# Optimization experiments

Hardware: AMD Instinct MI355X
Metric: run time of the kernel (lower is better)

The kernel has to match this reference:

```python
import jax, jax.numpy as jnp
import numpy as np

N_NODES = 32768
N_EDGES = 262144
B = 64
FT_IN = 256
HID = 256
HEADS = 4
C = HID // HEADS
FT_OUT = 256
NEG_SLOPE = 0.2


def _lin(k, fi, fo):
    return jax.random.normal(k, (fi, fo), dtype=jnp.float32) / np.sqrt(fi)


def setup_inputs() -> dict:
    key = jax.random.key(0)
    ks = jax.random.split(key, 20)
    x = jax.random.normal(ks[0], (N_NODES, FT_IN), dtype=jnp.float32)
    edge_index = jax.random.randint(ks[1], (2, N_EDGES), 0, N_NODES, dtype=jnp.int64)
    batch = jnp.repeat(jnp.arange(B, dtype=jnp.int64), N_NODES // B)  # sorted segment ids
    return {
        "x": x,
        "edge_index": edge_index,
        "batch": batch,
        "batch_size": B,
        "W1l": _lin(ks[2], FT_IN, HID),
        "W1r": _lin(ks[3], FT_IN, HID),
        "a1": jax.random.normal(ks[4], (HEADS, C), dtype=jnp.float32) / np.sqrt(C),
        "b1": jnp.zeros((HID,), dtype=jnp.float32),
        "W2l": _lin(ks[5], HID, HID),
        "W2r": _lin(ks[6], HID, HID),
        "a2": jax.random.normal(ks[7], (HEADS, C), dtype=jnp.float32) / np.sqrt(C),
        "b2": jnp.zeros((HID,), dtype=jnp.float32),
        "Wm1": _lin(ks[8], HID, 4 * HID),
        "bm1": jnp.zeros((4 * HID,), dtype=jnp.float32),
        "Wm2": _lin(ks[9], 4 * HID, HID),
        "bm2": jnp.zeros((HID,), dtype=jnp.float32),
        "Wf": _lin(ks[10], HID, FT_OUT),
        "bf": jnp.zeros((FT_OUT,), dtype=jnp.float32),
    }


def gatv2_layer(x, src, dst, Wl, Wr, att, bias):
    """PyG GATv2Conv (concat=True, add_self_loops=True, eval-mode dropout)."""
    n = x.shape[0]
    h, c = att.shape
    xl = (x @ Wl).reshape(n, h, c)  # source-side transform (x_j)
    xr = (x @ Wr).reshape(n, h, c)  # target-side transform (x_i)
    loop = jnp.arange(n, dtype=src.dtype)
    s = jnp.concatenate([src, loop])
    d = jnp.concatenate([dst, loop])
    # e_ij = a^T LeakyReLU(Wl x_j + Wr x_i), per head
    e = jax.nn.leaky_relu(xl[s] + xr[d], NEG_SLOPE)  # [E+N, H, C]
    score = jnp.einsum('ehc,hc->eh', e, att)  # [E+N, H]
    # segment softmax over incoming edges of each dst node
    m = jax.ops.segment_max(score, d, num_segments=n)
    ex = jnp.exp(score - m[d])
    denom = jax.ops.segment_sum(ex, d, num_segments=n)
    alpha = ex / denom[d]  # self-loops guarantee denom > 0
    out = jax.ops.segment_sum(alpha[..., None] * xl[s], d, num_segments=n)
    return out.reshape(n, h * c) + bias


def _gelu(x):
    return jax.nn.gelu(x, approximate=False)


def reference(x, edge_index, batch, batch_size,
              W1l, W1r, a1, b1, W2l, W2r, a2, b2,
              Wm1, bm1, Wm2, bm2, Wf, bf):
    src, dst = edge_index[0], edge_index[1]
    h = _gelu(gatv2_layer(x, src, dst, W1l, W1r, a1, b1))
    h = _gelu(gatv2_layer(h, src, dst, W2l, W2r, a2, b2))
    # global mean pool over graphs
    cnt = jax.ops.segment_sum(jnp.ones((h.shape[0],), h.dtype), batch, num_segments=batch_size)
    graph_mean = jax.ops.segment_sum(h, batch, num_segments=batch_size) / cnt[:, None]
    # root node of each graph (node 0 of each contiguous block)
    root = h.reshape(batch_size, -1, h.shape[-1])[:, 0, :]
    z = _gelu(root @ Wm1 + bm1)
    z = _gelu(z @ Wm2 + bm2)
    out = z @ Wf + bf
    return (out, graph_mean)
```

## Files before the change

kernel.cpp:

```cpp
#include <hip/hip_runtime.h>
#include <math.h>

#define NNODES 32768
#define BGRAPH 64
#define NPG 512
#define HID 256

typedef __bf16 bf16x8 __attribute__((ext_vector_type(8)));
typedef float f32x16 __attribute__((ext_vector_type(16)));
typedef unsigned short ushort_t;
typedef unsigned short ushort8v __attribute__((ext_vector_type(8)));
typedef unsigned short ushort4v __attribute__((ext_vector_type(4)));
typedef _Float16 half4v __attribute__((ext_vector_type(4)));

__device__ __forceinline__ float gelu_f(float x) {
  return 0.5f * x * (1.0f + erff(x * 0.70710678118654752440f));
}

__device__ __forceinline__ int swz_off(int r, int k) {
  int kblk = k & ~63;
  int ch = (k >> 3) & 7;
  int slot = ch ^ (r & 7);
  return r * 256 + kblk + (slot << 3) + (k & 7);
}

__device__ __forceinline__ void gll16(const void* g, void* l) {
  __builtin_amdgcn_global_load_lds(
      (const __attribute__((address_space(1))) unsigned int*)g,
      (__attribute__((address_space(3))) unsigned int*)l, 16, 0, 0);
}

__device__ __forceinline__ float dpp_sum16(float x) {
  int t;
  t = __builtin_amdgcn_update_dpp(0, __builtin_bit_cast(int, x), 0xB1, 0xF, 0xF, true);
  x += __builtin_bit_cast(float, t);
  t = __builtin_amdgcn_update_dpp(0, __builtin_bit_cast(int, x), 0x4E, 0xF, 0xF, true);
  x += __builtin_bit_cast(float, t);
  t = __builtin_amdgcn_update_dpp(0, __builtin_bit_cast(int, x), 0x141, 0xF, 0xF, true);
  x += __builtin_bit_cast(float, t);
  t = __builtin_amdgcn_update_dpp(0, __builtin_bit_cast(int, x), 0x140, 0xF, 0xF, true);
  x += __builtin_bit_cast(float, t);
  return x;
}

__global__ __launch_bounds__(256) void prep_kernel(
    const int* __restrict__ src, const int* __restrict__ dst, int E,
    int* __restrict__ cnt, ushort_t* __restrict__ col_pad,
    const float* __restrict__ W1l, const float* __restrict__ W1r,
    const float* __restrict__ W2l, const float* __restrict__ W2r,
    ushort_t* __restrict__ B1h, ushort_t* __restrict__ B1l,
    ushort_t* __restrict__ B2h, ushort_t* __restrict__ B2l,
    const float* __restrict__ x,
    ushort_t* __restrict__ Xh, ushort_t* __restrict__ Xl) {
  int b = blockIdx.x;
  if (b < 1024) {
    int e = b * 256 + threadIdx.x;
    if (e < E) {
      int d = dst[e];
      int slot = atomicAdd(&cnt[d], 1);
      if (slot < 64) col_pad[(d << 6) | slot] = (ushort_t)src[e];
    }
  } else if (b < 1152) {
    int idx = (b - 1024) * 256 + threadIdx.x;
    int layer = idx >> 14;
    int n = (idx >> 5) & 511;
    int c32 = idx & 31;
    const float* W = layer ? (n < 256 ? W2l : W2r) : (n < 256 ? W1l : W1r);
    int wn = n & 255;
    ushort8v hv, lv;
#pragma unroll
    for (int j = 0; j < 8; ++j) {
      float v = W[(size_t)(c32 * 8 + j) * 256 + wn];
      __bf16 h = (__bf16)v;
      float rem = v - (float)h;
      __bf16 l = (__bf16)rem;
      hv[j] = __builtin_bit_cast(ushort_t, h);
      lv[j] = __builtin_bit_cast(ushort_t, l);
    }
    int off = swz_off(n, c32 * 8);
    ushort_t* ho = layer ? B2h : B1h;
    ushort_t* lo = layer ? B2l : B1l;
    *(ushort8v*)(ho + off) = hv;
    *(ushort8v*)(lo + off) = lv;
  } else {
    int idx = (b - 1152) * 256 + threadIdx.x;
    int r = idx >> 5;
    int c32 = idx & 31;
    const float* srcp = x + (size_t)r * 256 + c32 * 8;
    float4 v0 = *(const float4*)srcp;
    float4 v1 = *(const float4*)(srcp + 4);
    float vv[8] = {v0.x, v0.y, v0.z, v0.w, v1.x, v1.y, v1.z, v1.w};
    ushort8v hv, lv;
#pragma unroll
    for (int j = 0; j < 8; ++j) {
      __bf16 h = (__bf16)vv[j];
      float rem = vv[j] - (float)h;
      __bf16 l = (__bf16)rem;
      hv[j] = __builtin_bit_cast(ushort_t, h);
      lv[j] = __builtin_bit_cast(ushort_t, l);
    }
    int off = swz_off(r, c32 * 8);
    *(ushort8v*)(Xh + off) = hv;
    *(ushort8v*)(Xl + off) = lv;
  }
}

__global__ __launch_bounds__(256, 2) void gemm_bf16x3(
    const ushort_t* __restrict__ Ahi, const ushort_t* __restrict__ Alo,
    const ushort_t* __restrict__ Bhi, const ushort_t* __restrict__ Blo,
    _Float16* __restrict__ Cl, float* __restrict__ Cr) {
  __shared__ ushort_t lds[4 * 128 * 64];
  int i = blockIdx.x;
  int xcd = i & 7, slot = i >> 3;
  int bm = (xcd * 32 + (slot >> 2)) * 128;
  int bn = (slot & 3) * 128;

  int tid = threadIdx.x;
  int w = tid >> 6, lane = tid & 63;
  int r = lane & 31, kg = lane >> 5;

  const ushort_t* gsrc = (w == 0) ? Ahi : (w == 1) ? Alo : (w == 2) ? Bhi : Blo;
  int rowbase = (w < 2) ? bm : bn;
  const ushort_t* gptr = gsrc + (size_t)(rowbase + (lane >> 3)) * 256 + (lane & 7) * 8;
  ushort_t* ldsw = lds + w * (128 * 64) + lane * 8;

  int wm0 = (w >> 1) * 64, wn0 = (w & 1) * 64;

  f32x16 acc[2][2];
#pragma unroll
  for (int mf = 0; mf < 2; ++mf)
#pragma unroll
    for (int nf = 0; nf < 2; ++nf)
#pragma unroll
      for (int e = 0; e < 16; ++e) acc[mf][nf][e] = 0.0f;

  for (int kk = 0; kk < 256; kk += 64) {
#pragma unroll
    for (int t = 0; t < 16; ++t)
      gll16(gptr + (size_t)t * 2048 + kk, ldsw + t * 512);
    __syncthreads();

#pragma unroll
    for (int ks = 0; ks < 4; ++ks) {
      int so = (((ks << 1) | kg) ^ (r & 7)) << 3;
      bf16x8 ah[2], al[2], bh[2], bl[2];
#pragma unroll
      for (int mf = 0; mf < 2; ++mf) {
        int rb = (wm0 + mf * 32 + r) * 64 + so;
        ah[mf] = *(const bf16x8*)(lds + rb);
        al[mf] = *(const bf16x8*)(lds + 8192 + rb);
      }
#pragma unroll
      for (int nf = 0; nf < 2; ++nf) {
        int rb = (wn0 + nf * 32 + r) * 64 + so;
        bh[nf] = *(const bf16x8*)(lds + 16384 + rb);
        bl[nf] = *(const bf16x8*)(lds + 24576 + rb);
      }
#pragma unroll
      for (int mf = 0; mf < 2; ++mf)
#pragma unroll
        for (int nf = 0; nf < 2; ++nf) {
          acc[mf][nf] = __builtin_amdgcn_mfma_f32_32x32x16_bf16(ah[mf], bh[nf], acc[mf][nf], 0, 0, 0);
          acc[mf][nf] = __builtin_amdgcn_mfma_f32_32x32x16_bf16(ah[mf], bl[nf], acc[mf][nf], 0, 0, 0);
          acc[mf][nf] = __builtin_amdgcn_mfma_f32_32x32x16_bf16(al[mf], bh[nf], acc[mf][nf], 0, 0, 0);
        }
    }
    __syncthreads();
  }

#pragma unroll
  for (int mf = 0; mf < 2; ++mf)
#pragma unroll
    for (int nf = 0; nf < 2; ++nf) {
      int colbase = bn + wn0 + nf * 32;
      int cn = (colbase + r) & 255;
#pragma unroll
      for (int g = 0; g < 16; ++g) {
        int row = bm + wm0 + mf * 32 + (g & 3) + ((g >> 2) << 3) + (kg << 2);
        if (colbase < 256)
          Cl[(size_t)row * 256 + cn] = (_Float16)acc[mf][nf][g];
        else
          Cr[(size_t)row * 256 + cn] = acc[mf][nf][g];
      }
    }
}

__global__ __launch_bounds__(256) void gat_agg(const _Float16* __restrict__ xl,
                                               const float* __restrict__ xr,
                                               const float* __restrict__ att,
                                               const float* __restrict__ bias,
                                               const int* __restrict__ cnt,
                                               const ushort_t* __restrict__ col_pad,
                                               ushort_t* __restrict__ hi_out,
                                               ushort_t* __restrict__ lo_out,
                                               _Float16* __restrict__ h2f16,
                                               float* __restrict__ rootbuf) {
  int wave = (int)((blockIdx.x * (size_t)blockDim.x + threadIdx.x) >> 6);
  int lane = threadIdx.x & 63;
  int d = wave;
  int c0 = lane * 4;
  float4 xr4 = *(const float4*)(xr + (size_t)d * HID + c0);
  float4 a4 = *(const float4*)(att + c0);
  int deg = cnt[d];
  deg = deg < 64 ? deg : 64;
  int mycol = (int)col_pad[(d << 6) + lane];

  auto loadrow = [&](int j) -> float4 {
    int s = (j < deg) ? __builtin_amdgcn_readlane(mycol, j) : d;
    half4v hv = *(const half4v*)(xl + (size_t)s * HID + c0);
    return make_float4((float)hv[0], (float)hv[1], (float)hv[2], (float)hv[3]);
  };

  float l = 0.f, A0 = 0.f, A1 = 0.f, A2 = 0.f, A3 = 0.f;
  float4 v = loadrow(0);
  for (int j = 0; j <= deg; ++j) {
    float4 vc = v;
    if (j < deg) v = loadrow(j + 1);
    float t0 = vc.x + xr4.x, t1 = vc.y + xr4.y, t2 = vc.z + xr4.z, t3 = vc.w + xr4.w;
    t0 = fmaf(0.4f, fabsf(t0), 0.6f * t0);
    t1 = fmaf(0.4f, fabsf(t1), 0.6f * t1);
    t2 = fmaf(0.4f, fabsf(t2), 0.6f * t2);
    t3 = fmaf(0.4f, fabsf(t3), 0.6f * t3);
    float sc = a4.x * t0;
    sc = fmaf(a4.y, t1, sc);
    sc = fmaf(a4.z, t2, sc);
    sc = fmaf(a4.w, t3, sc);
    sc = dpp_sum16(sc);
    float p = __expf(sc);
    l += p;
    A0 = fmaf(p, vc.x, A0);
    A1 = fmaf(p, vc.y, A1);
    A2 = fmaf(p, vc.z, A2);
    A3 = fmaf(p, vc.w, A3);
  }

  float inv = 1.0f / l;
  float v0 = gelu_f(fmaf(A0, inv, bias[c0 + 0]));
  float v1 = gelu_f(fmaf(A1, inv, bias[c0 + 1]));
  float v2 = gelu_f(fmaf(A2, inv, bias[c0 + 2]));
  float v3 = gelu_f(fmaf(A3, inv, bias[c0 + 3]));

  if (hi_out) {
    float vv[4] = {v0, v1, v2, v3};
    ushort4v hv, lv;
#pragma unroll
    for (int j = 0; j < 4; ++j) {
      __bf16 h = (__bf16)vv[j];
      float rem = vv[j] - (float)h;
      __bf16 lb = (__bf16)rem;
      hv[j] = __builtin_bit_cast(ushort_t, h);
      lv[j] = __builtin_bit_cast(ushort_t, lb);
    }
    int off = swz_off(d, c0);
    *(ushort4v*)(hi_out + off) = hv;
    *(ushort4v*)(lo_out + off) = lv;
  }
  if (h2f16) {
    half4v o;
    o[0] = (_Float16)v0; o[1] = (_Float16)v1; o[2] = (_Float16)v2; o[3] = (_Float16)v3;
    *(half4v*)(h2f16 + (size_t)d * HID + c0) = o;
    if ((d & (NPG - 1)) == 0)
      *(float4*)(rootbuf + (size_t)(d >> 9) * HID + c0) = make_float4(v0, v1, v2, v3);
  }
}

__global__ __launch_bounds__(256) void pool_kernel(const _Float16* __restrict__ h2,
                                                   float* __restrict__ gmean) {
  int g = blockIdx.x >> 2;
  int q = blockIdx.x & 3;
  int c = threadIdx.x;
  const _Float16* p = h2 + ((size_t)g * NPG + q * 128) * HID + c;
  float s = 0.f;
#pragma unroll 4
  for (int i = 0; i < 128; ++i) s += (float)p[(size_t)i * HID];
  atomicAdd(&gmean[(size_t)g * HID + c], s * (1.0f / (float)NPG));
}

template <int KIN, int NOUT, int NCHUNK, bool GELU>
__global__ __launch_bounds__(256) void mlp_kernel(const float* __restrict__ in, size_t row_stride,
                                                  const float* __restrict__ W,
                                                  const float* __restrict__ b,
                                                  float* __restrict__ outp) {
  __shared__ float s_in[KIN];
  int g = blockIdx.x / NCHUNK;
  int n0 = (blockIdx.x % NCHUNK) * (NOUT / NCHUNK);
  const float* row = in + (size_t)g * row_stride;
  for (int i = threadIdx.x; i < KIN; i += 256) s_in[i] = row[i];
  __syncthreads();
  constexpr int CPT = NOUT / NCHUNK / 256;
  float acc[CPT] = {};
  for (int k = 0; k < KIN; ++k) {
    float a = s_in[k];
#pragma unroll
    for (int j = 0; j < CPT; ++j) acc[j] += a * W[(size_t)k * NOUT + n0 + threadIdx.x + j * 256];
  }
#pragma unroll
  for (int j = 0; j < CPT; ++j) {
    float v = acc[j] + b[n0 + threadIdx.x + j * 256];
    if (GELU) v = gelu_f(v);
    outp[(size_t)g * NOUT + n0 + threadIdx.x + j * 256] = v;
  }
}

extern "C" void kernel_launch(void* const* d_in, const int* in_sizes, int n_in,
                              void* d_out, int out_size, void* d_ws, size_t ws_size,
                              hipStream_t stream) {
  const float* x   = (const float*)d_in[0];
  const int* edge  = (const int*)d_in[1];
  const float* W1l = (const float*)d_in[4];
  const float* W1r = (const float*)d_in[5];
  const float* a1  = (const float*)d_in[6];
  const float* b1  = (const float*)d_in[7];
  const float* W2l = (const float*)d_in[8];
  const float* W2r = (const float*)d_in[9];
  const float* a2  = (const float*)d_in[10];
  const float* b2  = (const float*)d_in[11];
  const float* Wm1 = (const float*)d_in[12];
  const float* bm1 = (const float*)d_in[13];
  const float* Wm2 = (const float*)d_in[14];
  const float* bm2 = (const float*)d_in[15];
  const float* Wf  = (const float*)d_in[16];
  const float* bf  = (const float*)d_in[17];
  float* out = (float*)d_out;
  float* gmean = out + BGRAPH * HID;

  const int n = NNODES;
  const int E = in_sizes[1] / 2;
  const int* src = edge;
  const int* dst = edge + E;

  ushort_t* R1h = (ushort_t*)d_ws;
  ushort_t* R1l = R1h + (size_t)n * 256;
  _Float16* h2f16 = (_Float16*)R1h;
  _Float16* xlh = (_Float16*)(R1l + (size_t)n * 256);
  float* xrbuf = (float*)(xlh + (size_t)n * 256);
  float* rootbuf = xrbuf + (size_t)n * 256;
  float* z1 = rootbuf + 64 * 256;
  float* z2 = z1 + 64 * 1024;
  ushort_t* B1h = (ushort_t*)(z2 + 64 * 256);
  ushort_t* B1l = B1h + 512 * 256;
  ushort_t* B2h = B1l + 512 * 256;
  ushort_t* B2l = B2h + 512 * 256;
  int* cnt = (int*)(B2l + 512 * 256);
  ushort_t* col_pad = (ushort_t*)(cnt + n);

  hipMemsetAsync(cnt, 0, (size_t)n * sizeof(int), stream);
  hipMemsetAsync(gmean, 0, (size_t)BGRAPH * HID * sizeof(float), stream);

  prep_kernel<<<1024 + 128 + 4096, 256, 0, stream>>>(
      src, dst, E, cnt, col_pad, W1l, W1r, W2l, W2r,
      B1h, B1l, B2h, B2l, x, R1h, R1l);

  gemm_bf16x3<<<1024, 256, 0, stream>>>(R1h, R1l, B1h, B1l, xlh, xrbuf);
  gat_agg<<<n / 4, 256, 0, stream>>>(xlh, xrbuf, a1, b1, cnt, col_pad,
                                     R1h, R1l, nullptr, nullptr);
  gemm_bf16x3<<<1024, 256, 0, stream>>>(R1h, R1l, B2h, B2l, xlh, xrbuf);
  gat_agg<<<n / 4, 256, 0, stream>>>(xlh, xrbuf, a2, b2, cnt, col_pad,
                                     nullptr, nullptr, h2f16, rootbuf);

  pool_kernel<<<BGRAPH * 4, 256, 0, stream>>>(h2f16, gmean);
  mlp_kernel<256, 1024, 4, true><<<BGRAPH * 4, 256, 0, stream>>>(rootbuf, 256, Wm1, bm1, z1);
  mlp_kernel<1024, 256, 1, true><<<BGRAPH, 256, 0, stream>>>(z1, 1024, Wm2, bm2, z2);
  mlp_kernel<256, 256, 1, false><<<BGRAPH, 256, 0, stream>>>(z2, 256, Wf, bf, out);
}
```

Baseline: 330.4 us.

## Store GEMM operands in MFMA fragment order and load directly from global

Producers now write the bf16 hi/lo operands in a layout that matches the MFMA 32x32x16 fragment order, so each lane loads its fragment with one contiguous 16-byte global read. The GEMM drops LDS staging, global_load_lds and the barriers, and raises launch bounds to 3 blocks per CU. This removes LDS traffic and sync, but each wave now reads its tiles from global/L2 with no sharing between waves in a block, which duplicates global traffic.

```diff
diff --git a/kernel.cpp b/kernel.cpp
--- a/kernel.cpp
+++ b/kernel.cpp
@@ -17,17 +17,9 @@
   return 0.5f * x * (1.0f + erff(x * 0.70710678118654752440f));
 }
 
-__device__ __forceinline__ int swz_off(int r, int k) {
-  int kblk = k & ~63;
-  int ch = (k >> 3) & 7;
-  int slot = ch ^ (r & 7);
-  return r * 256 + kblk + (slot << 3) + (k & 7);
-}
-
-__device__ __forceinline__ void gll16(const void* g, void* l) {
-  __builtin_amdgcn_global_load_lds(
-      (const __attribute__((address_space(1))) unsigned int*)g,
-      (__attribute__((address_space(3))) unsigned int*)l, 16, 0, 0);
+__device__ __forceinline__ size_t frag_off(int r, int k) {
+  return ((size_t)((r >> 5) * 16 + (k >> 4)) << 9) +
+         (size_t)(((r & 31) | (((k >> 3) & 1) << 5)) << 3) + (k & 7);
 }
 
 __device__ __forceinline__ float dpp_sum16(float x) {
@@ -77,7 +69,7 @@
       hv[j] = __builtin_bit_cast(ushort_t, h);
       lv[j] = __builtin_bit_cast(ushort_t, l);
     }
-    int off = swz_off(n, c32 * 8);
+    size_t off = frag_off(n, c32 * 8);
     ushort_t* ho = layer ? B2h : B1h;
     ushort_t* lo = layer ? B2l : B1l;
     *(ushort8v*)(ho + off) = hv;
@@ -99,32 +91,27 @@
       hv[j] = __builtin_bit_cast(ushort_t, h);
       lv[j] = __builtin_bit_cast(ushort_t, l);
     }
-    int off = swz_off(r, c32 * 8);
+    size_t off = frag_off(r, c32 * 8);
     *(ushort8v*)(Xh + off) = hv;
     *(ushort8v*)(Xl + off) = lv;
   }
 }
 
-__global__ __launch_bounds__(256, 2) void gemm_bf16x3(
+__global__ __launch_bounds__(256, 3) void gemm_bf16x3(
     const ushort_t* __restrict__ Ahi, const ushort_t* __restrict__ Alo,
     const ushort_t* __restrict__ Bhi, const ushort_t* __restrict__ Blo,
     _Float16* __restrict__ Cl, float* __restrict__ Cr) {
-  __shared__ ushort_t lds[4 * 128 * 64];
   int i = blockIdx.x;
   int xcd = i & 7, slot = i >> 3;
   int bm = (xcd * 32 + (slot >> 2)) * 128;
   int bn = (slot & 3) * 128;
 
-  int tid = threadIdx.x;
-  int w = tid >> 6, lane = tid & 63;
+  int w = threadIdx.x >> 6, lane = threadIdx.x & 63;
+  int wm0 = (w >> 1) * 64, wn0 = (w & 1) * 64;
   int r = lane & 31, kg = lane >> 5;
 
-  const ushort_t* gsrc = (w == 0) ? Ahi : (w == 1) ? Alo : (w == 2) ? Bhi : Blo;
-  int rowbase = (w < 2) ? bm : bn;
-  const ushort_t* gptr = gsrc + (size_t)(rowbase + (lane >> 3)) * 256 + (lane & 7) * 8;
-  ushort_t* ldsw = lds + w * (128 * 64) + lane * 8;
-
-  int wm0 = (w >> 1) * 64, wn0 = (w & 1) * 64;
+  int rb0 = (bm + wm0) >> 5;
+  int cb0 = (bn + wn0) >> 5;
 
   f32x16 acc[2][2];
 #pragma unroll
@@ -134,38 +121,29 @@
 #pragma unroll
       for (int e = 0; e < 16; ++e) acc[mf][nf][e] = 0.0f;
 
-  for (int kk = 0; kk < 256; kk += 64) {
-#pragma unroll
-    for (int t = 0; t < 16; ++t)
-      gll16(gptr + (size_t)t * 2048 + kk, ldsw + t * 512);
-    __syncthreads();
-
-#pragma unroll
-    for (int ks = 0; ks < 4; ++ks) {
-      int so = (((ks << 1) | kg) ^ (r & 7)) << 3;
-      bf16x8 ah[2], al[2], bh[2], bl[2];
-#pragma unroll
-      for (int mf = 0; mf < 2; ++mf) {
-        int rb = (wm0 + mf * 32 + r) * 64 + so;
-        ah[mf] = *(const bf16x8*)(lds + rb);
-        al[mf] = *(const bf16x8*)(lds + 8192 + rb);
+#pragma unroll
+  for (int kq = 0; kq < 16; ++kq) {
+    bf16x8 ah[2], al[2], bh[2], bl[2];
+#pragma unroll
+    for (int mf = 0; mf < 2; ++mf) {
+      size_t o = ((size_t)((rb0 + mf) * 16 + kq) << 9) + (lane << 3);
+      ah[mf] = *(const bf16x8*)(Ahi + o);
+      al[mf] = *(const bf16x8*)(Alo + o);
+    }
+#pragma unroll
+    for (int nf = 0; nf < 2; ++nf) {
+      size_t o = ((size_t)((cb0 + nf) * 16 + kq) << 9) + (lane << 3);
+      bh[nf] = *(const bf16x8*)(Bhi + o);
+      bl[nf] = *(const bf16x8*)(Blo + o);
+    }
+#pragma unroll
+    for (int mf = 0; mf < 2; ++mf)
+#pragma unroll
+      for (int nf = 0; nf < 2; ++nf) {
+        acc[mf][nf] = __builtin_amdgcn_mfma_f32_32x32x16_bf16(ah[mf], bh[nf], acc[mf][nf], 0, 0, 0);
+        acc[mf][nf] = __builtin_amdgcn_mfma_f32_32x32x16_bf16(ah[mf], bl[nf], acc[mf][nf], 0, 0, 0);
+        acc[mf][nf] = __builtin_amdgcn_mfma_f32_32x32x16_bf16(al[mf], bh[nf], acc[mf][nf], 0, 0, 0);
       }
-#pragma unroll
-      for (int nf = 0; nf < 2; ++nf) {
-        int rb = (wn0 + nf * 32 + r) * 64 + so;
-        bh[nf] = *(const bf16x8*)(lds + 16384 + rb);
-        bl[nf] = *(const bf16x8*)(lds + 24576 + rb);
-      }
-#pragma unroll
-      for (int mf = 0; mf < 2; ++mf)
-#pragma unroll
-        for (int nf = 0; nf < 2; ++nf) {
-          acc[mf][nf] = __builtin_amdgcn_mfma_f32_32x32x16_bf16(ah[mf], bh[nf], acc[mf][nf], 0, 0, 0);
-          acc[mf][nf] = __builtin_amdgcn_mfma_f32_32x32x16_bf16(ah[mf], bl[nf], acc[mf][nf], 0, 0, 0);
-          acc[mf][nf] = __builtin_amdgcn_mfma_f32_32x32x16_bf16(al[mf], bh[nf], acc[mf][nf], 0, 0, 0);
-        }
-    }
-    __syncthreads();
   }
 
 #pragma unroll
@@ -251,7 +229,7 @@
       hv[j] = __builtin_bit_cast(ushort_t, h);
       lv[j] = __builtin_bit_cast(ushort_t, lb);
     }
-    int off = swz_off(d, c0);
+    size_t off = frag_off(d, c0);
     *(ushort4v*)(hi_out + off) = hv;
     *(ushort4v*)(lo_out + off) = lv;
   }
```

Result: no change. 329.9 us (-0.1%).

## Load GEMM weights as pre-laid MFMA fragments from global; fuse pool and MLP tail

Applied to the files above, without the earlier changes.

The weight matrices are now stored in an MFMA-fragment layout during prep. The GEMM reads the B operand straight from global (L2-resident) instead of staging it in LDS. This halves LDS use per block and raises the occupancy target to 3 blocks per SM. Separately, pooling now reduces inside a 1024-thread block without atomics, which removes the gmean memset, and the last two MLP layers are fused into one kernel to save a launch. The trade-off is that direct global B loads add latency inside the MFMA loop.

```diff
diff --git a/kernel.cpp b/kernel.cpp
--- a/kernel.cpp
+++ b/kernel.cpp
@@ -22,6 +22,11 @@
   int ch = (k >> 3) & 7;
   int slot = ch ^ (r & 7);
   return r * 256 + kblk + (slot << 3) + (k & 7);
+}
+
+__device__ __forceinline__ size_t frag_off(int r, int k) {
+  return ((size_t)((r >> 5) * 16 + (k >> 4)) << 9) +
+         (size_t)(((r & 31) | (((k >> 3) & 1) << 5)) << 3) + (k & 7);
 }
 
 __device__ __forceinline__ void gll16(const void* g, void* l) {
@@ -77,7 +82,7 @@
       hv[j] = __builtin_bit_cast(ushort_t, h);
       lv[j] = __builtin_bit_cast(ushort_t, l);
     }
-    int off = swz_off(n, c32 * 8);
+    size_t off = frag_off(n, c32 * 8);
     ushort_t* ho = layer ? B2h : B1h;
     ushort_t* lo = layer ? B2l : B1l;
     *(ushort8v*)(ho + off) = hv;
@@ -105,11 +110,11 @@
   }
 }
 
-__global__ __launch_bounds__(256, 2) void gemm_bf16x3(
+__global__ __launch_bounds__(256, 3) void gemm_bf16x3(
     const ushort_t* __restrict__ Ahi, const ushort_t* __restrict__ Alo,
     const ushort_t* __restrict__ Bhi, const ushort_t* __restrict__ Blo,
     _Float16* __restrict__ Cl, float* __restrict__ Cr) {
-  __shared__ ushort_t lds[4 * 128 * 64];
+  __shared__ ushort_t lds[2 * 8192];
   int i = blockIdx.x;
   int xcd = i & 7, slot = i >> 3;
   int bm = (xcd * 32 + (slot >> 2)) * 128;
@@ -117,14 +122,9 @@
 
   int tid = threadIdx.x;
   int w = tid >> 6, lane = tid & 63;
+  int wm0 = (w >> 1) * 64, wn0 = (w & 1) * 64;
   int r = lane & 31, kg = lane >> 5;
-
-  const ushort_t* gsrc = (w == 0) ? Ahi : (w == 1) ? Alo : (w == 2) ? Bhi : Blo;
-  int rowbase = (w < 2) ? bm : bn;
-  const ushort_t* gptr = gsrc + (size_t)(rowbase + (lane >> 3)) * 256 + (lane & 7) * 8;
-  ushort_t* ldsw = lds + w * (128 * 64) + lane * 8;
-
-  int wm0 = (w >> 1) * 64, wn0 = (w & 1) * 64;
+  int cb0 = (bn + wn0) >> 5;
 
   f32x16 acc[2][2];
 #pragma unroll
@@ -136,10 +136,16 @@
 
   for (int kk = 0; kk < 256; kk += 64) {
 #pragma unroll
-    for (int t = 0; t < 16; ++t)
-      gll16(gptr + (size_t)t * 2048 + kk, ldsw + t * 512);
+    for (int t = 0; t < 8; ++t) {
+      int tile = t >> 2;
+      int q = tid + (t & 3) * 256;
+      const ushort_t* gsrc = tile ? Alo : Ahi;
+      gll16(gsrc + (size_t)(bm + (q >> 3)) * 256 + kk + (q & 7) * 8,
+            lds + tile * 8192 + q * 8);
+    }
     __syncthreads();
 
+    int kq0 = kk >> 4;
 #pragma unroll
     for (int ks = 0; ks < 4; ++ks) {
       int so = (((ks << 1) | kg) ^ (r & 7)) << 3;
@@ -152,9 +158,9 @@
       }
 #pragma unroll
       for (int nf = 0; nf < 2; ++nf) {
-        int rb = (wn0 + nf * 32 + r) * 64 + so;
-        bh[nf] = *(const bf16x8*)(lds + 16384 + rb);
-        bl[nf] = *(const bf16x8*)(lds + 24576 + rb);
+        size_t o = ((size_t)((cb0 + nf) * 16 + kq0 + ks) << 9) + (lane << 3);
+        bh[nf] = *(const bf16x8*)(Bhi + o);
+        bl[nf] = *(const bf16x8*)(Blo + o);
       }
 #pragma unroll
       for (int mf = 0; mf < 2; ++mf)
@@ -264,42 +270,61 @@
   }
 }
 
-__global__ __launch_bounds__(256) void pool_kernel(const _Float16* __restrict__ h2,
-                                                   float* __restrict__ gmean) {
-  int g = blockIdx.x >> 2;
-  int q = blockIdx.x & 3;
-  int c = threadIdx.x;
+__global__ __launch_bounds__(1024) void pool_kernel(const _Float16* __restrict__ h2,
+                                                    float* __restrict__ gmean) {
+  __shared__ float buf[1024];
+  int g = blockIdx.x;
+  int q = threadIdx.x >> 8;
+  int c = threadIdx.x & 255;
   const _Float16* p = h2 + ((size_t)g * NPG + q * 128) * HID + c;
   float s = 0.f;
 #pragma unroll 4
   for (int i = 0; i < 128; ++i) s += (float)p[(size_t)i * HID];
-  atomicAdd(&gmean[(size_t)g * HID + c], s * (1.0f / (float)NPG));
-}
-
-template <int KIN, int NOUT, int NCHUNK, bool GELU>
-__global__ __launch_bounds__(256) void mlp_kernel(const float* __restrict__ in, size_t row_stride,
-                                                  const float* __restrict__ W,
-                                                  const float* __restrict__ b,
-                                                  float* __restrict__ outp) {
-  __shared__ float s_in[KIN];
-  int g = blockIdx.x / NCHUNK;
-  int n0 = (blockIdx.x % NCHUNK) * (NOUT / NCHUNK);
-  const float* row = in + (size_t)g * row_stride;
-  for (int i = threadIdx.x; i < KIN; i += 256) s_in[i] = row[i];
+  buf[threadIdx.x] = s;
   __syncthreads();
-  constexpr int CPT = NOUT / NCHUNK / 256;
-  float acc[CPT] = {};
-  for (int k = 0; k < KIN; ++k) {
-    float a = s_in[k];
-#pragma unroll
-    for (int j = 0; j < CPT; ++j) acc[j] += a * W[(size_t)k * NOUT + n0 + threadIdx.x + j * 256];
-  }
-#pragma unroll
-  for (int j = 0; j < CPT; ++j) {
-    float v = acc[j] + b[n0 + threadIdx.x + j * 256];
-    if (GELU) v = gelu_f(v);
-    outp[(size_t)g * NOUT + n0 + threadIdx.x + j * 256] = v;
-  }
+  if (threadIdx.x < 256) {
+    float tot = buf[c] + buf[256 + c] + buf[512 + c] + buf[768 + c];
+    gmean[(size_t)g * HID + c] = tot * (1.0f / (float)NPG);
+  }
+}
+
+__global__ __launch_bounds__(256) void mlp1_kernel(const float* __restrict__ in,
+                                                   const float* __restrict__ W,
+                                                   const float* __restrict__ b,
+                                                   float* __restrict__ outp) {
+  __shared__ float s_in[256];
+  int g = blockIdx.x >> 2;
+  int n0 = (blockIdx.x & 3) * 256;
+  const float* row = in + (size_t)g * 256;
+  s_in[threadIdx.x] = row[threadIdx.x];
+  __syncthreads();
+  float acc = 0.f;
+  for (int k = 0; k < 256; ++k)
+    acc = fmaf(s_in[k], W[(size_t)k * 1024 + n0 + threadIdx.x], acc);
+  outp[(size_t)g * 1024 + n0 + threadIdx.x] = gelu_f(acc + b[n0 + threadIdx.x]);
+}
+
+__global__ __launch_bounds__(256) void mlp23_kernel(const float* __restrict__ z1,
+                                                    const float* __restrict__ Wm2,
+                                                    const float* __restrict__ bm2,
+                                                    const float* __restrict__ Wf,
+                                                    const float* __restrict__ bf,
+                                                    float* __restrict__ outp) {
+  __shared__ float s1[1024];
+  __shared__ float s2[256];
+  int g = blockIdx.x;
+  int c = threadIdx.x;
+  const float* row = z1 + (size_t)g * 1024;
+#pragma unroll
+  for (int i = 0; i < 4; ++i) s1[c + i * 256] = row[c + i * 256];
+  __syncthreads();
+  float acc = 0.f;
+  for (int k = 0; k < 1024; ++k) acc = fmaf(s1[k], Wm2[(size_t)k * 256 + c], acc);
+  s2[c] = gelu_f(acc + bm2[c]);
+  __syncthreads();
+  float acc2 = 0.f;
+  for (int k = 0; k < 256; ++k) acc2 = fmaf(s2[k], Wf[(size_t)k * 256 + c], acc2);
+  outp[(size_t)g * 256 + c] = acc2 + bf[c];
 }
 
 extern "C" void kernel_launch(void* const* d_in, const int* in_sizes, int n_in,
@@ -336,8 +361,7 @@
   float* xrbuf = (float*)(xlh + (size_t)n * 256);
   float* rootbuf = xrbuf + (size_t)n * 256;
   float* z1 = rootbuf + 64 * 256;
-  float* z2 = z1 + 64 * 1024;
-  ushort_t* B1h = (ushort_t*)(z2 + 64 * 256);
+  ushort_t* B1h = (ushort_t*)(z1 + 64 * 1024);
   ushort_t* B1l = B1h + 512 * 256;
   ushort_t* B2h = B1l + 512 * 256;
   ushort_t* B2l = B2h + 512 * 256;
@@ -345,7 +369,6 @@
   ushort_t* col_pad = (ushort_t*)(cnt + n);
 
   hipMemsetAsync(cnt, 0, (size_t)n * sizeof(int), stream);
-  hipMemsetAsync(gmean, 0, (size_t)BGRAPH * HID * sizeof(float), stream);
 
   prep_kernel<<<1024 + 128 + 4096, 256, 0, stream>>>(
       src, dst, E, cnt, col_pad, W1l, W1r, W2l, W2r,
@@ -358,8 +381,7 @@
   gat_agg<<<n / 4, 256, 0, stream>>>(xlh, xrbuf, a2, b2, cnt, col_pad,
                                      nullptr, nullptr, h2f16, rootbuf);
 
-  pool_kernel<<<BGRAPH * 4, 256, 0, stream>>>(h2f16, gmean);
-  mlp_kernel<256, 1024, 4, true><<<BGRAPH * 4, 256, 0, stream>>>(rootbuf, 256, Wm1, bm1, z1);
-  mlp_kernel<1024, 256, 1, true><<<BGRAPH, 256, 0, stream>>>(z1, 1024, Wm2, bm2, z2);
-  mlp_kernel<256, 256, 1, false><<<BGRAPH, 256, 0, stream>>>(z2, 256, Wf, bf, out);
-}
+  pool_kernel<<<BGRAPH, 1024, 0, stream>>>(h2f16, gmean);
+  mlp1_kernel<<<BGRAPH * 4, 256, 0, stream>>>(rootbuf, Wm1, bm1, z1);
+  mlp23_kernel<<<BGRAPH, 256, 0, stream>>>(z1, Wm2, bm2, Wf, bf, out);
+}
```

Measured after the change: 336.6 us. About the same (+1.9%).
